# Kernel optimization log

Hardware: AMD Instinct MI355X
Metric: run time of the kernel (lower is better)

The kernel has to match this reference:

```python
import jax, jax.numpy as jnp
import numpy as np

L, B, T, N, M = 2, 32, 256, 1024, 1024  # layers, batch, time, input feat, hidden


def setup_inputs() -> dict:
    key = jax.random.key(0)
    ks = jax.random.split(key, 7)
    s = 0.02  # weight init scale
    return {
        "x": jax.random.normal(ks[0], (B, T, N), dtype=jnp.float32),
        "h": jax.random.normal(ks[1], (L, B, M), dtype=jnp.float32) * 0.1,
        "c": jax.random.normal(ks[2], (L, B, M), dtype=jnp.float32) * 0.1,
        "Wih": jax.random.normal(ks[3], (L, 4 * M, N), dtype=jnp.float32) * s,
        "Whh": jax.random.normal(ks[4], (L, 4 * M, M), dtype=jnp.float32) * s,
        "bih": jnp.zeros((L, 4 * M), dtype=jnp.float32),
        "bhh": jnp.zeros((L, 4 * M), dtype=jnp.float32),
    }


def _lstm_cell(x_t, h_t, c_t, Wih_l, Whh_l, b_l):
    # gates: [i | f | g | o], matching torch.nn.LSTMCell layout
    gates = x_t @ Wih_l.T + h_t @ Whh_l.T + b_l  # (B, 4M)
    i, f, g, o = jnp.split(gates, 4, axis=-1)
    i, f, o = jax.nn.sigmoid(i), jax.nn.sigmoid(f), jax.nn.sigmoid(o)
    c_new = f * c_t + i * jnp.tanh(g)
    h_new = o * jnp.tanh(c_new)
    return h_new, c_new


def reference(x, h, c, Wih, Whh, bih, bhh):
    b_sum = bih + bhh  # (L, 4M)

    def step(carry, x_t):
        h_cur, c_cur = carry  # each (L, B, M)
        hs, cs = [], []
        inp = x_t
        for l in range(L):  # small fixed layer loop
            h_l, c_l = _lstm_cell(inp, h_cur[l], c_cur[l], Wih[l], Whh[l], b_sum[l])
            hs.append(h_l)
            cs.append(c_l)
            inp = h_l
        return (jnp.stack(hs, 0), jnp.stack(cs, 0)), inp  # emit top-layer h

    (h_final, c_final), outs_tbm = jax.lax.scan(step, (h, c), jnp.swapaxes(x, 0, 1))
    outs = jnp.swapaxes(outs_tbm, 0, 1)  # (B, T, M)
    return outs, h_final, c_final
```

## Files before the change

kernel.cpp:

```cpp
#include <hip/hip_runtime.h>


typedef __bf16 bf16x8 __attribute__((ext_vector_type(8)));
typedef float  f32x4  __attribute__((ext_vector_type(4)));
typedef unsigned u32x4 __attribute__((ext_vector_type(4)));

__device__ __forceinline__ unsigned short f2bf(float f) {
    union { float f; unsigned u; } v; v.f = f;
    unsigned u = v.u;
    unsigned r = u + 0x7fffu + ((u >> 16) & 1u);
    return (unsigned short)(r >> 16);
}
__device__ __forceinline__ float sigmoidf_fast(float x) {
    return 1.0f / (1.0f + __expf(-x));
}
__device__ __forceinline__ float tanhf_fast(float x) {
    return 1.0f - 2.0f / (__expf(2.0f * x) + 1.0f);
}

__global__ void cvt_w_concat(const float* __restrict__ src,
                             unsigned short* __restrict__ dst, int off, int n4) {
    int i = blockIdx.x * blockDim.x + threadIdx.x;
    int stride = gridDim.x * blockDim.x;
    for (; i < n4; i += stride) {
        float4 v = ((const float4*)src)[i];
        ushort4 o;
        o.x = f2bf(v.x); o.y = f2bf(v.y); o.z = f2bf(v.z); o.w = f2bf(v.w);
        int row = i >> 8;
        int c4  = i & 255;
        *(ushort4*)&dst[(size_t)row * 2048 + off + c4 * 4] = o;
    }
}

__global__ void cvt_x_tiles(const float* __restrict__ x,
                            unsigned short* __restrict__ xT) {
    int t = blockIdx.x, tid = threadIdx.x;
    unsigned short* tile = xT + (size_t)t * 32768;
    for (int b = 0; b < 32; ++b) {
        float4 v = *(const float4*)&x[((size_t)b * 256 + t) * 1024 + tid * 4];
        ushort4 o;
        o.x = f2bf(v.x); o.y = f2bf(v.y); o.z = f2bf(v.z); o.w = f2bf(v.w);
        *(ushort4*)&tile[(tid >> 2) * 512 + b * 16 + (tid & 3) * 4] = o;
    }
}

__global__ void cvt_h0_tiles(const float* __restrict__ h0,
                             unsigned short* __restrict__ h0T) {
    int l = blockIdx.x, tid = threadIdx.x;
    unsigned short* tile = h0T + (size_t)l * 32768;
    for (int b = 0; b < 32; ++b) {
        float4 v = *(const float4*)&h0[((size_t)l * 32 + b) * 1024 + tid * 4];
        ushort4 o;
        o.x = f2bf(v.x); o.y = f2bf(v.y); o.z = f2bf(v.z); o.w = f2bf(v.w);
        *(ushort4*)&tile[(tid >> 2) * 512 + b * 16 + (tid & 3) * 4] = o;
    }
}

__global__ void out_transpose(const float* __restrict__ outT,
                              float* __restrict__ out) {
    int t = blockIdx.x, tid = threadIdx.x;
    const float* tile = outT + (size_t)t * 32768;
    for (int b = 0; b < 32; ++b) {
        float4 v = *(const float4*)&tile[(tid >> 2) * 512 + b * 16 + (tid & 3) * 4];
        *(float4*)&out[((size_t)b * 256 + t) * 1024 + tid * 4] = v;
    }
}

__device__ __forceinline__ void pollge(const unsigned* fp, unsigned tgt) {
    while (true) {
        unsigned v = __hip_atomic_load(fp, __ATOMIC_RELAXED,
                                       __HIP_MEMORY_SCOPE_AGENT);
        if (__all((int)(v >= tgt))) break;
        __builtin_amdgcn_s_sleep(1);
    }
}

#define STAGE_LOADS(PTR, ARR, FLAGS_STR) \
    _Pragma("unroll") \
    for (int si = 0; si < 16; si++) \
        asm volatile("global_load_dwordx4 %0, %1, off" FLAGS_STR \
                     : "=v"(ARR[si]) : "v"(PTR + si * 4096) : "memory");

__global__ __launch_bounds__(256, 1) void lstm_fused(
    const unsigned short* __restrict__ Wcat,
    const unsigned short* __restrict__ xT,
    unsigned short* __restrict__ seqT,
    const unsigned short* __restrict__ h0T,
    unsigned short* __restrict__ hparT,
    float* __restrict__ outT,
    const float* __restrict__ c0,
    const float* __restrict__ bih, const float* __restrict__ bhh,
    float* __restrict__ out, unsigned int* flags)
{
    __shared__ __align__(16) unsigned short bufH[32][1024];
    __shared__ __align__(16) unsigned short bufX[32][1024];
    __shared__ __align__(16) unsigned short hout_bf[32][16];
    __shared__ __align__(16) float hout_f[32][16];

    const int tid  = threadIdx.x;
    const int lane = tid & 63;
    const int w    = tid >> 6;
    const int l    = blockIdx.x >> 6;
    const int bidl = blockIdx.x & 63;
    const int m0   = bidl * 16;
    const int n    = lane & 15;
    const int g    = lane >> 4;
    const int lk   = g * 8;
    const int nn7  = n & 7;

    bf16x8 wx[32], wh[32];
    const unsigned short* Wl = Wcat + (size_t)l * 4096 * 2048;
    #pragma unroll
    for (int ct = 0; ct < 4; ct++) {
        int vc = ct * 16 + n;
        size_t jrow = (size_t)((vc & 3) * 1024 + m0 + (vc >> 2));
        #pragma unroll
        for (int kc = 0; kc < 8; kc++) {
            wx[ct*8+kc] = *(const bf16x8*)&Wl[jrow*2048 +        w*256 + kc*32 + lk];
            wh[ct*8+kc] = *(const bf16x8*)&Wl[jrow*2048 + 1024 + w*256 + kc*32 + lk];
        }
    }

    const int eb = lane >> 1;
    const int q  = lane & 1;
    const int em = m0 + 4 * w + 2 * q;
    float bs0[4], bs1[4];
    #pragma unroll
    for (int gg = 0; gg < 4; gg++) {
        bs0[gg] = bih[l*4096 + gg*1024 + em]     + bhh[l*4096 + gg*1024 + em];
        bs1[gg] = bih[l*4096 + gg*1024 + em + 1] + bhh[l*4096 + gg*1024 + em + 1];
    }
    float2 creg = *(const float2*)&c0[(size_t)l * 32768 + eb * 1024 + em];
    float2 hlast = {0.f, 0.f};
    const int uh = eb >> 4, urow = eb & 15;

    char* const bH = (char*)&bufH[0][0];
    char* const bX = (char*)&bufX[0][0];
    const int sb = (tid >> 1) & 31;
    const int stOff = sb * 2048 + ((w * 32 + (tid & 1) * 16) ^ ((sb & 7) << 4));

    typedef float GredT[2][4][16][20];
    GredT* gred = (GredT*)bH;

    const int hb64 = (nn7 >> 2) * 64;
    const int gx16 = (g ^ (nn7 & 3)) * 16;
    const int rOffA0 = n * 2048 + w * 512 + gx16 + hb64;
    const int rOffA1 = n * 2048 + w * 512 + gx16 + (64 - hb64);

    f32x4 acc0[4] = {}, acc1[4] = {};

    auto gemmbuf = [&](const char* base, const bf16x8* wf) {
        const char* pA0 = base + rOffA0;
        const char* pA1 = base + rOffA1;
        const char* pB0 = pA0 + 16 * 2048;
        const char* pB1 = pA1 + 16 * 2048;
        #pragma unroll
        for (int kc2 = 0; kc2 < 4; kc2++) {
            bf16x8 a0 = *(const bf16x8*)(pA0 + kc2 * 128);
            bf16x8 a1 = *(const bf16x8*)(pB0 + kc2 * 128);
            #pragma unroll
            for (int ct = 0; ct < 4; ct++) {
                acc0[ct] = __builtin_amdgcn_mfma_f32_16x16x32_bf16(a0, wf[ct*8+2*kc2], acc0[ct], 0,0,0);
                acc1[ct] = __builtin_amdgcn_mfma_f32_16x16x32_bf16(a1, wf[ct*8+2*kc2], acc1[ct], 0,0,0);
            }
            bf16x8 b0 = *(const bf16x8*)(pA1 + kc2 * 128);
            bf16x8 b1 = *(const bf16x8*)(pB1 + kc2 * 128);
            #pragma unroll
            for (int ct = 0; ct < 4; ct++) {
                acc0[ct] = __builtin_amdgcn_mfma_f32_16x16x32_bf16(b0, wf[ct*8+2*kc2+1], acc0[ct], 0,0,0);
                acc1[ct] = __builtin_amdgcn_mfma_f32_16x16x32_bf16(b1, wf[ct*8+2*kc2+1], acc1[ct], 0,0,0);
            }
        }
    };

    auto stageX = [&](const char* tb, bool byp) {
        u32x4 hv[16];
        const char* gp = tb + tid * 16;
        if (byp) { STAGE_LOADS(gp, hv, " sc0 sc1") }
        else     { STAGE_LOADS(gp, hv, "") }
        asm volatile("s_waitcnt vmcnt(0)" ::: "memory");
        #pragma unroll
        for (int si = 0; si < 16; si++)
            *(u32x4*)(bX + stOff + si * 128) = hv[si];
    };

    if (l == 0) stageX((const char*)xT, false);
    __syncthreads();

    const int lag = l * 2;
    #pragma unroll 1
    for (int s = 0; s < 258; s++) {
        const int  t   = s - lag;
        const bool act = (t >= 0) && (t < 256);

        if (act) {
            const char* hbase = (t == 0)
                ? (const char*)(h0T + (size_t)l * 32768)
                : (l == 0 ? (const char*)(seqT + (size_t)(t - 1) * 32768)
                          : (const char*)(hparT + (size_t)((t - 1) & 1) * 32768));
            u32x4 hv[16];
            {
                const char* gp = hbase + tid * 16;
                STAGE_LOADS(gp, hv, " sc0 sc1")
            }
            __builtin_amdgcn_sched_barrier(0);

            #pragma unroll
            for (int ct = 0; ct < 4; ct++) {
                acc0[ct] = (f32x4){0.f, 0.f, 0.f, 0.f};
                acc1[ct] = (f32x4){0.f, 0.f, 0.f, 0.f};
            }
            gemmbuf(bX, wx);

            asm volatile("s_waitcnt vmcnt(0)" ::: "memory");
            __builtin_amdgcn_sched_barrier(0);
            #pragma unroll
            for (int si = 0; si < 16; si++)
                *(u32x4*)(bH + stOff + si * 128) = hv[si];
            __syncthreads();
            gemmbuf(bH, wh);
            __syncthreads();
            {
                int r0 = g * 4;
                #pragma unroll
                for (int ct = 0; ct < 4; ct++) {
                    *(f32x4*)&gred[w][0][ct][n][r0] = acc0[ct];
                    *(f32x4*)&gred[w][1][ct][n][r0] = acc1[ct];
                }
            }
            __syncthreads();
            float g8[8];
            #pragma unroll
            for (int j = 0; j < 8; j++) {
                g8[j] = (gred[0][uh][w][8*q+j][urow] + gred[1][uh][w][8*q+j][urow])
                      + (gred[2][uh][w][8*q+j][urow] + gred[3][uh][w][8*q+j][urow]);
            }
            float gi0 = g8[0] + bs0[0], gf0 = g8[1] + bs0[1];
            float gg0 = g8[2] + bs0[2], go0 = g8[3] + bs0[3];
            float gi1 = g8[4] + bs1[0], gf1 = g8[5] + bs1[1];
            float gg1 = g8[6] + bs1[2], go1 = g8[7] + bs1[3];

            float c0n = sigmoidf_fast(gf0) * creg.x + sigmoidf_fast(gi0) * tanhf_fast(gg0);
            float c1n = sigmoidf_fast(gf1) * creg.y + sigmoidf_fast(gi1) * tanhf_fast(gg1);
            float h0v = sigmoidf_fast(go0) * tanhf_fast(c0n);
            float h1v = sigmoidf_fast(go1) * tanhf_fast(c1n);
            creg.x = c0n; creg.y = c1n;
            hlast.x = h0v; hlast.y = h1v;

            unsigned hp = (unsigned)f2bf(h0v) | ((unsigned)f2bf(h1v) << 16);
            *(unsigned*)&hout_bf[eb][4*w + 2*q] = hp;
            if (l == 1) {
                float2 hv2 = {h0v, h1v};
                *(float2*)&hout_f[eb][4*w + 2*q] = hv2;
            }
            __syncthreads();
            if (tid < 64) {
                u32x4 v = *(const u32x4*)((const char*)&hout_bf[0][0] + tid * 16);
                const char* dp = (l == 0)
                    ? (const char*)(seqT  + (size_t)t * 32768)       + bidl * 1024 + tid * 16
                    : (const char*)(hparT + (size_t)(t & 1) * 32768) + bidl * 1024 + tid * 16;
                asm volatile("global_store_dwordx4 %0, %1, off sc0 sc1"
                             :: "v"(dp), "v"(v) : "memory");
                asm volatile("s_waitcnt vmcnt(0)" ::: "memory");
                if (tid == 0)
                    __hip_atomic_store(flags + l * 64 + bidl, (unsigned)(s + 1),
                                       __ATOMIC_RELAXED, __HIP_MEMORY_SCOPE_AGENT);
            } else if (l == 1 && tid < 192) {
                int u = tid - 64;
                f32x4 v = *(const f32x4*)((const char*)&hout_f[0][0] + u * 16);
                *(f32x4*)((char*)outT + (size_t)t * 131072 + bidl * 2048 + u * 16) = v;
            }
        } else if (tid == 0) {
            __hip_atomic_store(flags + l * 64 + bidl, (unsigned)(s + 1),
                               __ATOMIC_RELAXED, __HIP_MEMORY_SCOPE_AGENT);
        }

        const int  tn   = t + 1;
        const bool xact = (tn >= ((l == 0) ? 1 : 0)) && (tn <= 255);
        if (xact) {
            stageX(l == 0 ? (const char*)(xT   + (size_t)tn * 32768)
                          : (const char*)(seqT + (size_t)tn * 32768), l == 1);
        }

        if (tid < 128) pollge(flags + tid, (unsigned)(s + 1));
        __syncthreads();
    }

    float* hF = out + (size_t)8192 * 1024 + (size_t)l * 32768;
    float* cF = out + (size_t)8192 * 1024 + 65536 + (size_t)l * 32768;
    float2 hf2 = {hlast.x, hlast.y};
    *(float2*)&hF[eb * 1024 + em] = hf2;
    float2 cf2 = {creg.x, creg.y};
    *(float2*)&cF[eb * 1024 + em] = cf2;
}

extern "C" void kernel_launch(void* const* d_in, const int* in_sizes, int n_in,
                              void* d_out, int out_size, void* d_ws, size_t ws_size,
                              hipStream_t stream)
{
    const float* x   = (const float*)d_in[0];
    const float* h0  = (const float*)d_in[1];
    const float* c0  = (const float*)d_in[2];
    const float* Wih = (const float*)d_in[3];
    const float* Whh = (const float*)d_in[4];
    const float* bih = (const float*)d_in[5];
    const float* bhh = (const float*)d_in[6];
    float* out = (float*)d_out;

    char* p = (char*)d_ws;
    unsigned short* xT    = (unsigned short*)p; p += (size_t)256 * 32768 * 2;
    unsigned short* seqT  = (unsigned short*)p; p += (size_t)256 * 32768 * 2;
    unsigned short* Wcat  = (unsigned short*)p; p += (size_t)2 * 4096 * 2048 * 2;
    unsigned short* h0T   = (unsigned short*)p; p += (size_t)2 * 32768 * 2;
    unsigned short* hparT = (unsigned short*)p; p += (size_t)2 * 32768 * 2;
    float*          outT  = (float*)p;          p += (size_t)256 * 32768 * 4;
    unsigned int*   flags = (unsigned int*)p;   p += 4096;

    hipMemsetAsync(flags, 0, 4096, stream);
    cvt_w_concat<<<1024, 256, 0, stream>>>(Wih, Wcat, 0,    2 * 4096 * 256);
    cvt_w_concat<<<1024, 256, 0, stream>>>(Whh, Wcat, 1024, 2 * 4096 * 256);
    cvt_x_tiles<<<256, 256, 0, stream>>>(x, xT);
    cvt_h0_tiles<<<2, 256, 0, stream>>>(h0, h0T);

    lstm_fused<<<128, 256, 0, stream>>>(Wcat, xT, seqT, h0T, hparT, outT,
                                        c0, bih, bhh, out, flags);

    out_transpose<<<256, 256, 0, stream>>>(outT, out);
}
```

Baseline: 1.569 ms.

## Double block size and split x/h GEMM halves across separate waves

Launches 512 threads per block. Half of the waves run the input-weight GEMM from the x buffer and the other half run the recurrent GEMM from the h buffer, each holding only 32 weight fragments instead of 64. Partial sums from 8 waves are reduced through LDS and each thread computes one hidden element. This halves register pressure per thread and adds waves to hide latency. The cost is that the h load no longer overlaps the x GEMM, plus an extra barrier and a larger reduction.

```diff
diff --git a/kernel.cpp b/kernel.cpp
--- a/kernel.cpp
+++ b/kernel.cpp
@@ -75,13 +75,13 @@
     }
 }
 
-#define STAGE_LOADS(PTR, ARR, FLAGS_STR) \
+#define STAGE_LOADS8(ARR, PTR, FLAGS_STR) \
     _Pragma("unroll") \
-    for (int si = 0; si < 16; si++) \
+    for (int si = 0; si < 8; si++) \
         asm volatile("global_load_dwordx4 %0, %1, off" FLAGS_STR \
-                     : "=v"(ARR[si]) : "v"(PTR + si * 4096) : "memory");
-
-__global__ __launch_bounds__(256, 1) void lstm_fused(
+                     : "=v"(ARR[si]) : "v"(PTR + si * 8192) : "memory");
+
+__global__ __launch_bounds__(512, 2) void lstm_fused(
     const unsigned short* __restrict__ Wcat,
     const unsigned short* __restrict__ xT,
     unsigned short* __restrict__ seqT,
@@ -92,14 +92,15 @@
     const float* __restrict__ bih, const float* __restrict__ bhh,
     float* __restrict__ out, unsigned int* flags)
 {
-    __shared__ __align__(16) unsigned short bufH[32][1024];
-    __shared__ __align__(16) unsigned short bufX[32][1024];
+    __shared__ __align__(16) char pool[131072];
     __shared__ __align__(16) unsigned short hout_bf[32][16];
     __shared__ __align__(16) float hout_f[32][16];
 
     const int tid  = threadIdx.x;
     const int lane = tid & 63;
     const int w    = tid >> 6;
+    const int half = w & 1;
+    const int kw   = w >> 1;
     const int l    = blockIdx.x >> 6;
     const int bidl = blockIdx.x & 63;
     const int m0   = bidl * 16;
@@ -108,48 +109,58 @@
     const int lk   = g * 8;
     const int nn7  = n & 7;
 
-    bf16x8 wx[32], wh[32];
+    char* const bH = pool;
+    char* const bX = pool + 65536;
+    float* const gred = (float*)pool;
+#define GIDX(wv,bh,ct,nn,r) ((((((wv)*2+(bh))*4+(ct))*16+(nn))*20)+(r))
+
+    bf16x8 wf[32];
     const unsigned short* Wl = Wcat + (size_t)l * 4096 * 2048;
     #pragma unroll
     for (int ct = 0; ct < 4; ct++) {
         int vc = ct * 16 + n;
         size_t jrow = (size_t)((vc & 3) * 1024 + m0 + (vc >> 2));
         #pragma unroll
-        for (int kc = 0; kc < 8; kc++) {
-            wx[ct*8+kc] = *(const bf16x8*)&Wl[jrow*2048 +        w*256 + kc*32 + lk];
-            wh[ct*8+kc] = *(const bf16x8*)&Wl[jrow*2048 + 1024 + w*256 + kc*32 + lk];
-        }
-    }
-
-    const int eb = lane >> 1;
-    const int q  = lane & 1;
-    const int em = m0 + 4 * w + 2 * q;
-    float bs0[4], bs1[4];
+        for (int kc = 0; kc < 8; kc++)
+            wf[ct*8+kc] = *(const bf16x8*)
+                &Wl[jrow*2048 + half*1024 + kw*256 + kc*32 + lk];
+    }
+
+    const int eb  = tid >> 4;
+    const int sub = tid & 15;
+    const int em  = m0 + sub;
+    float bs[4];
     #pragma unroll
-    for (int gg = 0; gg < 4; gg++) {
-        bs0[gg] = bih[l*4096 + gg*1024 + em]     + bhh[l*4096 + gg*1024 + em];
-        bs1[gg] = bih[l*4096 + gg*1024 + em + 1] + bhh[l*4096 + gg*1024 + em + 1];
-    }
-    float2 creg = *(const float2*)&c0[(size_t)l * 32768 + eb * 1024 + em];
-    float2 hlast = {0.f, 0.f};
+    for (int gg = 0; gg < 4; gg++)
+        bs[gg] = bih[l*4096 + gg*1024 + em] + bhh[l*4096 + gg*1024 + em];
+    float creg  = c0[(size_t)l * 32768 + eb * 1024 + em];
+    float hlast = 0.f;
     const int uh = eb >> 4, urow = eb & 15;
-
-    char* const bH = (char*)&bufH[0][0];
-    char* const bX = (char*)&bufX[0][0];
+    const int ctr = sub >> 2, nb = (sub & 3) * 4;
+
     const int sb = (tid >> 1) & 31;
-    const int stOff = sb * 2048 + ((w * 32 + (tid & 1) * 16) ^ ((sb & 7) << 4));
-
-    typedef float GredT[2][4][16][20];
-    GredT* gred = (GredT*)bH;
+    const int stOff = sb * 2048
+                    + ((w * 32 + (tid & 1) * 16) ^ ((sb & 7) << 4));
 
     const int hb64 = (nn7 >> 2) * 64;
     const int gx16 = (g ^ (nn7 & 3)) * 16;
-    const int rOffA0 = n * 2048 + w * 512 + gx16 + hb64;
-    const int rOffA1 = n * 2048 + w * 512 + gx16 + (64 - hb64);
-
-    f32x4 acc0[4] = {}, acc1[4] = {};
-
-    auto gemmbuf = [&](const char* base, const bf16x8* wf) {
+    const int rOffA0 = n * 2048 + kw * 512 + gx16 + hb64;
+    const int rOffA1 = n * 2048 + kw * 512 + gx16 + (64 - hb64);
+
+    f32x4 acc0[4], acc1[4];
+
+    auto stage = [&](char* dst, const char* tb, bool byp) {
+        u32x4 hv[8];
+        const char* gp = tb + tid * 16;
+        if (byp) { STAGE_LOADS8(hv, gp, " sc0 sc1") }
+        else     { STAGE_LOADS8(hv, gp, "") }
+        asm volatile("s_waitcnt vmcnt(0)" ::: "memory");
+        #pragma unroll
+        for (int si = 0; si < 8; si++)
+            *(u32x4*)(dst + stOff + si * 256) = hv[si];
+    };
+
+    auto gemmbuf = [&](const char* base) {
         const char* pA0 = base + rOffA0;
         const char* pA1 = base + rOffA1;
         const char* pB0 = pA0 + 16 * 2048;
@@ -173,18 +184,7 @@
         }
     };
 
-    auto stageX = [&](const char* tb, bool byp) {
-        u32x4 hv[16];
-        const char* gp = tb + tid * 16;
-        if (byp) { STAGE_LOADS(gp, hv, " sc0 sc1") }
-        else     { STAGE_LOADS(gp, hv, "") }
-        asm volatile("s_waitcnt vmcnt(0)" ::: "memory");
-        #pragma unroll
-        for (int si = 0; si < 16; si++)
-            *(u32x4*)(bX + stOff + si * 128) = hv[si];
-    };
-
-    if (l == 0) stageX((const char*)xT, false);
+    if (l == 0) stage(bX, (const char*)xT, false);
     __syncthreads();
 
     const int lag = l * 2;
@@ -194,66 +194,48 @@
         const bool act = (t >= 0) && (t < 256);
 
         if (act) {
-            const char* hbase = (t == 0)
+            const char* hb = (t == 0)
                 ? (const char*)(h0T + (size_t)l * 32768)
                 : (l == 0 ? (const char*)(seqT + (size_t)(t - 1) * 32768)
                           : (const char*)(hparT + (size_t)((t - 1) & 1) * 32768));
-            u32x4 hv[16];
-            {
-                const char* gp = hbase + tid * 16;
-                STAGE_LOADS(gp, hv, " sc0 sc1")
-            }
-            __builtin_amdgcn_sched_barrier(0);
+            stage(bH, hb, true);
+            __syncthreads();
 
             #pragma unroll
             for (int ct = 0; ct < 4; ct++) {
                 acc0[ct] = (f32x4){0.f, 0.f, 0.f, 0.f};
                 acc1[ct] = (f32x4){0.f, 0.f, 0.f, 0.f};
             }
-            gemmbuf(bX, wx);
-
-            asm volatile("s_waitcnt vmcnt(0)" ::: "memory");
-            __builtin_amdgcn_sched_barrier(0);
-            #pragma unroll
-            for (int si = 0; si < 16; si++)
-                *(u32x4*)(bH + stOff + si * 128) = hv[si];
+            gemmbuf(half ? bH : bX);
             __syncthreads();
-            gemmbuf(bH, wh);
-            __syncthreads();
+
             {
                 int r0 = g * 4;
                 #pragma unroll
                 for (int ct = 0; ct < 4; ct++) {
-                    *(f32x4*)&gred[w][0][ct][n][r0] = acc0[ct];
-                    *(f32x4*)&gred[w][1][ct][n][r0] = acc1[ct];
+                    *(f32x4*)&gred[GIDX(w, 0, ct, n, r0)] = acc0[ct];
+                    *(f32x4*)&gred[GIDX(w, 1, ct, n, r0)] = acc1[ct];
                 }
             }
             __syncthreads();
-            float g8[8];
+
+            float s0 = 0.f, s1 = 0.f, s2 = 0.f, s3 = 0.f;
             #pragma unroll
-            for (int j = 0; j < 8; j++) {
-                g8[j] = (gred[0][uh][w][8*q+j][urow] + gred[1][uh][w][8*q+j][urow])
-                      + (gred[2][uh][w][8*q+j][urow] + gred[3][uh][w][8*q+j][urow]);
-            }
-            float gi0 = g8[0] + bs0[0], gf0 = g8[1] + bs0[1];
-            float gg0 = g8[2] + bs0[2], go0 = g8[3] + bs0[3];
-            float gi1 = g8[4] + bs1[0], gf1 = g8[5] + bs1[1];
-            float gg1 = g8[6] + bs1[2], go1 = g8[7] + bs1[3];
-
-            float c0n = sigmoidf_fast(gf0) * creg.x + sigmoidf_fast(gi0) * tanhf_fast(gg0);
-            float c1n = sigmoidf_fast(gf1) * creg.y + sigmoidf_fast(gi1) * tanhf_fast(gg1);
-            float h0v = sigmoidf_fast(go0) * tanhf_fast(c0n);
-            float h1v = sigmoidf_fast(go1) * tanhf_fast(c1n);
-            creg.x = c0n; creg.y = c1n;
-            hlast.x = h0v; hlast.y = h1v;
-
-            unsigned hp = (unsigned)f2bf(h0v) | ((unsigned)f2bf(h1v) << 16);
-            *(unsigned*)&hout_bf[eb][4*w + 2*q] = hp;
-            if (l == 1) {
-                float2 hv2 = {h0v, h1v};
-                *(float2*)&hout_f[eb][4*w + 2*q] = hv2;
-            }
+            for (int wv = 0; wv < 8; wv++) {
+                s0 += gred[GIDX(wv, uh, ctr, nb + 0, urow)];
+                s1 += gred[GIDX(wv, uh, ctr, nb + 1, urow)];
+                s2 += gred[GIDX(wv, uh, ctr, nb + 2, urow)];
+                s3 += gred[GIDX(wv, uh, ctr, nb + 3, urow)];
+            }
+            float gi = s0 + bs[0], gf = s1 + bs[1];
+            float gg = s2 + bs[2], go = s3 + bs[3];
+            float cn = sigmoidf_fast(gf) * creg + sigmoidf_fast(gi) * tanhf_fast(gg);
+            float hn = sigmoidf_fast(go) * tanhf_fast(cn);
+            creg = cn; hlast = hn;
+            hout_bf[eb][sub] = f2bf(hn);
+            if (l == 1) hout_f[eb][sub] = hn;
             __syncthreads();
+
             if (tid < 64) {
                 u32x4 v = *(const u32x4*)((const char*)&hout_bf[0][0] + tid * 16);
                 const char* dp = (l == 0)
@@ -277,10 +259,9 @@
 
         const int  tn   = t + 1;
         const bool xact = (tn >= ((l == 0) ? 1 : 0)) && (tn <= 255);
-        if (xact) {
-            stageX(l == 0 ? (const char*)(xT   + (size_t)tn * 32768)
-                          : (const char*)(seqT + (size_t)tn * 32768), l == 1);
-        }
+        if (xact)
+            stage(bX, l == 0 ? (const char*)(xT   + (size_t)tn * 32768)
+                             : (const char*)(seqT + (size_t)tn * 32768), l == 1);
 
         if (tid < 128) pollge(flags + tid, (unsigned)(s + 1));
         __syncthreads();
@@ -288,10 +269,8 @@
 
     float* hF = out + (size_t)8192 * 1024 + (size_t)l * 32768;
     float* cF = out + (size_t)8192 * 1024 + 65536 + (size_t)l * 32768;
-    float2 hf2 = {hlast.x, hlast.y};
-    *(float2*)&hF[eb * 1024 + em] = hf2;
-    float2 cf2 = {creg.x, creg.y};
-    *(float2*)&cF[eb * 1024 + em] = cf2;
+    hF[eb * 1024 + em] = hlast;
+    cF[eb * 1024 + em] = creg;
 }
 
 extern "C" void kernel_launch(void* const* d_in, const int* in_sizes, int n_in,
@@ -322,7 +301,7 @@
     cvt_x_tiles<<<256, 256, 0, stream>>>(x, xT);
     cvt_h0_tiles<<<2, 256, 0, stream>>>(h0, h0T);
 
-    lstm_fused<<<128, 256, 0, stream>>>(Wcat, xT, seqT, h0T, hparT, outT,
+    lstm_fused<<<128, 512, 0, stream>>>(Wcat, xT, seqT, h0T, hparT, outT,
                                         c0, bih, bhh, out, flags);
 
     out_transpose<<<256, 256, 0, stream>>>(outT, out);
```

Result: slower. 2.423 ms (+54.4%).
